# Kernel optimization log

Measured on AMD Instinct MI355X. Metric: run time of the kernel, lower is better.

Reference implementation:

```python
import jax, jax.numpy as jnp
import numpy as np

B, N, DIM = 8, 8192, 512
H, DH = 8, 64
INNER = H * DH
EPS = 1e-5


def setup_inputs() -> dict:
    key = jax.random.key(0)
    ks = jax.random.split(key, 5)
    x = jax.random.normal(ks[0], (B, N, DIM), dtype=jnp.float32)
    w_qkv = jax.random.normal(ks[1], (DIM, 3 * INNER), dtype=jnp.float32) * (DIM ** -0.5)
    ln_w = jnp.ones((INNER,), dtype=jnp.float32)
    ln_b = jnp.zeros((INNER,), dtype=jnp.float32)
    w_out = jax.random.normal(ks[2], (INNER, DIM), dtype=jnp.float32) * (INNER ** -0.5)
    b_out = jnp.zeros((DIM,), dtype=jnp.float32)
    return {"x": x, "w_qkv": w_qkv, "ln_w": ln_w, "ln_b": ln_b,
            "w_out": w_out, "b_out": b_out}


def _layernorm(x, w, b):
    mu = jnp.mean(x, axis=-1, keepdims=True)
    var = jnp.mean(jnp.square(x - mu), axis=-1, keepdims=True)
    return (x - mu) * jax.lax.rsqrt(var + EPS) * w + b


def reference(x, w_qkv, ln_w, ln_b, w_out, b_out):
    b, n, _ = x.shape
    qkv = x @ w_qkv  # [b, n, 3*inner]
    q, k, v = jnp.split(qkv, 3, axis=-1)
    # b n (h d) -> b h n d
    def heads(t):
        return t.reshape(b, n, H, DH).transpose(0, 2, 1, 3)
    q, k, v = heads(q), heads(k), heads(v)
    q = jax.nn.relu(q)
    k = jax.nn.relu(k)
    kv = jnp.einsum('bhnm,bhnd->bhmd', k, v)   # [b, h, d, d]
    out = jnp.einsum('bhnm,bhmd->bhnd', q, kv)  # [b, h, n, d]
    out = out.transpose(0, 2, 1, 3).reshape(b, n, INNER)
    out = _layernorm(out, ln_w, ln_b)
    return out @ w_out + b_out
```

## Files before the change

### kernel.cpp

```cpp
#include <hip/hip_runtime.h>
#include <stdint.h>

#define B_ 8
#define N_ 8192
#define DIM_ 512
#define H_ 8
#define DH_ 64
#define ROWS (B_*N_)
#define TRIPLE (3*DIM_)
#define EPS_ 1e-5f

typedef __attribute__((ext_vector_type(8))) short short8;
typedef __attribute__((ext_vector_type(4))) float f32x4;
typedef __attribute__((ext_vector_type(4))) float fl4;
typedef __attribute__((ext_vector_type(4))) unsigned short us4;
typedef __attribute__((ext_vector_type(8))) unsigned short us8;

#define AS1 __attribute__((address_space(1)))
#define AS3 __attribute__((address_space(3)))

__device__ __forceinline__ void gld16(const void* g, void* l) {
    __builtin_amdgcn_global_load_lds((const AS1 void*)(uintptr_t)g,
                                     (AS3 void*)(unsigned)(uintptr_t)l, 16, 0, 0);
}

__device__ inline unsigned short f2bf(float f) {
    union { float f; unsigned int u; } x; x.f = f;
    unsigned int r = x.u + 0x7fffu + ((x.u >> 16) & 1u);
    return (unsigned short)(r >> 16);
}
__device__ inline float bf2f(unsigned short b) {
    union { unsigned int u; float f; } x; x.u = ((unsigned int)b) << 16;
    return x.f;
}

__device__ __forceinline__ int eoff(int row, int col) {
    return row * 64 + (col ^ ((((unsigned)row >> 2) & 3) << 4));
}

__global__ __launch_bounds__(256) void k_cvt(const float* __restrict__ x,
                                             unsigned short* __restrict__ xb) {
    size_t i = ((size_t)blockIdx.x * 256 + threadIdx.x) * 8;
    fl4 a = *(const fl4*)(x + i);
    fl4 b = *(const fl4*)(x + i + 4);
    us8 r;
    r[0] = f2bf(a[0]); r[1] = f2bf(a[1]); r[2] = f2bf(a[2]); r[3] = f2bf(a[3]);
    r[4] = f2bf(b[0]); r[5] = f2bf(b[1]); r[6] = f2bf(b[2]); r[7] = f2bf(b[3]);
    *(us8*)(xb + i) = r;
}

__global__ __launch_bounds__(256) void k_prep(const float* __restrict__ wq,
        const float* __restrict__ wo,
        unsigned short* __restrict__ wqT, unsigned short* __restrict__ woT) {
    __shared__ float T[32][33];
    int bid = blockIdx.x;
    const float* src; unsigned short* dst; int srcCols, dstCols, k0, n0;
    if (bid < 768) {
        int tn = bid % 48, tk = bid / 48;
        src = wq; dst = wqT; srcCols = 1536; dstCols = 512;
        k0 = tk * 32; n0 = tn * 32;
    } else {
        int b = bid - 768;
        int tn = b % 16, tk = b / 16;
        src = wo; dst = woT; srcCols = 512; dstCols = 512;
        k0 = tk * 32; n0 = tn * 32;
    }
    int t = threadIdx.x, r = t >> 3, c4 = (t & 7) * 4;
    fl4 v = *(const fl4*)(src + (size_t)(k0 + r) * srcCols + n0 + c4);
    T[c4 + 0][r] = v[0]; T[c4 + 1][r] = v[1];
    T[c4 + 2][r] = v[2]; T[c4 + 3][r] = v[3];
    __syncthreads();
    us4 o;
    o[0] = f2bf(T[r][c4 + 0]); o[1] = f2bf(T[r][c4 + 1]);
    o[2] = f2bf(T[r][c4 + 2]); o[3] = f2bf(T[r][c4 + 3]);
    *(us4*)(dst + (size_t)(n0 + r) * dstCols + k0 + c4) = o;
}

__global__ __launch_bounds__(512, 2) void k_qkv8(const unsigned short* __restrict__ xb,
        const unsigned short* __restrict__ wT,
        unsigned short* __restrict__ qkv)
{
    __shared__ __align__(1024) unsigned short Ab[4][8192];
    __shared__ __align__(1024) unsigned short Bb[4][8192];

    const int tid  = threadIdx.x;
    const int lane = tid & 63;
    const int wid  = tid >> 6;
    const int wr   = wid >> 2;
    const int wc   = wid & 3;
    const int lr   = lane & 15;

    int id  = blockIdx.x;
    int nid = (id & 7) * 192 + (id >> 3);
    int n0  = (nid % 6) * 256;
    int m0  = (nid / 6) * 256;

    const unsigned short* pA[2];
    const unsigned short* pB[2];
    unsigned ldst[2];
#pragma unroll
    for (int j = 0; j < 2; ++j) {
        int s    = tid + j * 512;
        int row  = ((s >> 6) << 4) + ((s >> 2) & 15);
        int colb = ((s & 3) << 4) ^ (((s >> 5) & 1) << 5);
        int col  = colb >> 1;
        pA[j] = xb + (size_t)(m0 + row) * 512 + col;
        pB[j] = wT + (size_t)(n0 + row) * 512 + col;
        ldst[j] = (unsigned)((j * 512 + wid * 64) * 8);
    }
    const int kg = (lane >> 4) * 8;
    const int lo = lr * 32 + (kg ^ ((lr >> 3) << 4));

    auto STAGE = [&](int t, int slot) {
#pragma unroll
        for (int j = 0; j < 2; ++j) {
            gld16(pA[j] + t * 32, (void*)&Ab[slot][ldst[j]]);
            gld16(pB[j] + t * 32, (void*)&Bb[slot][ldst[j]]);
        }
    };

    f32x4 acc[8][4] = {};
    short8 af[8], bfr[4];

    STAGE(0, 0);
    STAGE(1, 1);
    STAGE(2, 2);

#define WAITV(n) asm volatile("s_waitcnt vmcnt(" #n ")" ::: "memory")
#pragma unroll
    for (int t = 0; t < 16; ++t) {
        if (t <= 13)      WAITV(8);
        else if (t == 14) WAITV(4);
        else              WAITV(0);
        __builtin_amdgcn_s_barrier();
        __builtin_amdgcn_sched_barrier(0);

        if (t + 3 < 16) STAGE(t + 3, (t + 3) & 3);
        const unsigned short* Ac = Ab[t & 3];
        const unsigned short* Bc = Bb[t & 3];
#pragma unroll
        for (int m = 0; m < 8; ++m)
            af[m] = *(const short8*)&Ac[(wr * 8 + m) * 512 + lo];
#pragma unroll
        for (int n = 0; n < 4; ++n)
            bfr[n] = *(const short8*)&Bc[(wc * 4 + n) * 512 + lo];

        __builtin_amdgcn_s_setprio(1);
#pragma unroll
        for (int m = 0; m < 8; ++m)
#pragma unroll
            for (int n = 0; n < 4; ++n)
                acc[m][n] = __builtin_amdgcn_mfma_f32_16x16x32_bf16(af[m], bfr[n], acc[m][n], 0, 0, 0);
        __builtin_amdgcn_s_setprio(0);
    }
#undef WAITV

    __syncthreads();

    unsigned short* S = (wid < 4) ? (&Ab[0][0] + wid * 8192)
                                  : (&Bb[0][0] + (wid - 4) * 8192);
    const bool relu_tile = (n0 < 1024);
#pragma unroll
    for (int m = 0; m < 8; ++m) {
        int rbase = m * 16 + ((lane >> 4) << 2);
#pragma unroll
        for (int n = 0; n < 4; ++n) {
            int col = n * 16 + lr;
#pragma unroll
            for (int r = 0; r < 4; ++r) {
                float v = acc[m][n][r];
                if (relu_tile && v < 0.0f) v = 0.0f;
                S[eoff(rbase + r, col)] = f2bf(v);
            }
        }
    }
    __syncthreads();
    {
        int rsub = lane >> 3, sub = lane & 7;
        size_t grow = (size_t)(m0 + wr * 128);
        int gcol = n0 + wc * 64 + sub * 8;
#pragma unroll
        for (int rd = 0; rd < 16; ++rd) {
            int row = rd * 8 + rsub;
            short8 vv = *(const short8*)&S[eoff(row, sub * 8)];
            *(short8*)(qkv + (grow + row) * TRIPLE + gcol) = vv;
        }
    }
}

__global__ __launch_bounds__(256) void k_qkv_f(const float* __restrict__ x,
        const unsigned short* __restrict__ wT,
        unsigned short* __restrict__ qkv)
{
    __shared__ unsigned short As[128][40];
    __shared__ unsigned short Bs[128][40];
    int t = threadIdx.x;
    int lane = t & 63, wave = t >> 6;
    int m0 = blockIdx.y * 128;
    int n0 = blockIdx.x * 128;
    int wm = (wave & 1) * 64, wn = (wave >> 1) * 64;
    int lr = lane & 15, kg = (lane >> 4) * 8;

    f32x4 acc[4][4] = {};
    for (int k0 = 0; k0 < DIM_; k0 += 32) {
#pragma unroll
        for (int i = 0; i < 4; ++i) {
            int c = t + 256 * i;
            int r = c >> 3, c4 = (c & 7) * 4;
            fl4 v = *(const fl4*)(x + (size_t)(m0 + r) * DIM_ + k0 + c4);
            unsigned short* dst = &As[r][c4];
            dst[0] = f2bf(v[0]); dst[1] = f2bf(v[1]); dst[2] = f2bf(v[2]); dst[3] = f2bf(v[3]);
        }
#pragma unroll
        for (int i = 0; i < 2; ++i) {
            int c = t + 256 * i;
            int r = c >> 2, c8 = (c & 3) * 8;
            *(int4*)&Bs[r][c8] = *(const int4*)(wT + (size_t)(n0 + r) * DIM_ + k0 + c8);
        }
        __syncthreads();
        short8 af[4], bfr[4];
#pragma unroll
        for (int i = 0; i < 4; ++i) af[i]  = *(short8*)&As[wm + i*16 + lr][kg];
#pragma unroll
        for (int j = 0; j < 4; ++j) bfr[j] = *(short8*)&Bs[wn + j*16 + lr][kg];
#pragma unroll
        for (int i = 0; i < 4; ++i)
#pragma unroll
            for (int j = 0; j < 4; ++j)
                acc[i][j] = __builtin_amdgcn_mfma_f32_16x16x32_bf16(af[i], bfr[j], acc[i][j], 0, 0, 0);
        __syncthreads();
    }
#pragma unroll
    for (int i = 0; i < 4; ++i) {
        int row = m0 + wm + i*16 + (lane >> 4) * 4;
#pragma unroll
        for (int j = 0; j < 4; ++j) {
            int col = n0 + wn + j*16 + (lane & 15);
            bool rl = (col < 1024);
#pragma unroll
            for (int r = 0; r < 4; ++r) {
                float v = acc[i][j][r];
                if (rl && v < 0.0f) v = 0.0f;
                qkv[(size_t)(row + r) * TRIPLE + col] = f2bf(v);
            }
        }
    }
}

__global__ __launch_bounds__(256) void k_kv(const unsigned short* __restrict__ qkv,
                                            float* __restrict__ kv)
{
    __shared__ unsigned short KT[64][136];
    __shared__ unsigned short VT[64][136];
    __shared__ float red[64 * 64];
    int t = threadIdx.x, lane = t & 63, wave = t >> 6;
    int bh = blockIdx.x;
    int b = bh >> 3, h = bh & 7;
    int chunk = blockIdx.y;
    size_t rowbase = (size_t)b * N_ + (size_t)chunk * 1024;
    int kcol = DIM_ + h * 64;
    int vcol = 2 * DIM_ + h * 64;
    int lr = lane & 15;

    f32x4 acc[4][4] = {};
    for (int tile = 0; tile < 8; ++tile) {
        size_t r0 = rowbase + tile * 128;
#pragma unroll
        for (int i = 0; i < 8; ++i) {
            int c = t + 256 * i;
            int r = c >> 4, f4 = (c & 15) * 4;
            us4 kq = *(const us4*)(qkv + (r0 + r) * TRIPLE + kcol + f4);
            us4 vq = *(const us4*)(qkv + (r0 + r) * TRIPLE + vcol + f4);
#pragma unroll
            for (int j = 0; j < 4; ++j) { KT[f4 + j][r] = kq[j]; VT[f4 + j][r] = vq[j]; }
        }
        __syncthreads();
        int kg = wave * 32 + (lane >> 4) * 8;
        short8 af[4], bfr[4];
#pragma unroll
        for (int i = 0; i < 4; ++i) af[i]  = *(short8*)&KT[i*16 + lr][kg];
#pragma unroll
        for (int j = 0; j < 4; ++j) bfr[j] = *(short8*)&VT[j*16 + lr][kg];
#pragma unroll
        for (int i = 0; i < 4; ++i)
#pragma unroll
            for (int j = 0; j < 4; ++j)
                acc[i][j] = __builtin_amdgcn_mfma_f32_16x16x32_bf16(af[i], bfr[j], acc[i][j], 0, 0, 0);
        __syncthreads();
    }
    for (int w = 0; w < 4; ++w) {
        if (wave == w) {
#pragma unroll
            for (int i = 0; i < 4; ++i)
#pragma unroll
                for (int j = 0; j < 4; ++j)
#pragma unroll
                    for (int r = 0; r < 4; ++r) {
                        int m = i*16 + (lane >> 4) * 4 + r;
                        int d = j*16 + (lane & 15);
                        if (w == 0) red[m * 64 + d] = acc[i][j][r];
                        else        red[m * 64 + d] += acc[i][j][r];
                    }
        }
        __syncthreads();
    }
    float* kvout = kv + (size_t)bh * 4096;
#pragma unroll
    for (int i = 0; i < 16; ++i) {
        int idx = t + 256 * i;
        atomicAdd(&kvout[idx], red[idx]);
    }
}

__global__ __launch_bounds__(256) void k_attn(unsigned short* __restrict__ qkv,
                                              const float* __restrict__ kv,
                                              float* __restrict__ rowstats)
{
    __shared__ unsigned short Qh[128][72];
    __shared__ unsigned short kvT[64][72];
    __shared__ __align__(64) unsigned short Sout[128 * 64];
    int t = threadIdx.x, lane = t & 63, wave = t >> 6;
    size_t r0 = (size_t)blockIdx.x * 128;
    int b = (int)(r0 / N_);
    int lr = lane & 15;

    float s8[8] = {}, ss8[8] = {};

    for (int h = 0; h < H_; ++h) {
#pragma unroll
        for (int i = 0; i < 8; ++i) {
            int c = t + 256 * i;
            int r = c >> 4, f4 = (c & 15) * 4;
            *(us4*)&Qh[r][f4] = *(const us4*)(qkv + (r0 + r) * TRIPLE + h * 64 + f4);
        }
        const float* kvh = kv + (size_t)(b * 8 + h) * 4096;
#pragma unroll
        for (int i = 0; i < 16; ++i) {
            int idx = t + 256 * i;
            int m = idx >> 6, d = idx & 63;
            kvT[d][m] = f2bf(kvh[idx]);
        }
        __syncthreads();
        f32x4 acc[2][4] = {};
#pragma unroll
        for (int ks = 0; ks < 2; ++ks) {
            int kg = ks * 32 + (lane >> 4) * 8;
            short8 af[2], bfr[4];
#pragma unroll
            for (int i = 0; i < 2; ++i) af[i]  = *(short8*)&Qh[wave*32 + i*16 + lr][kg];
#pragma unroll
            for (int j = 0; j < 4; ++j) bfr[j] = *(short8*)&kvT[j*16 + lr][kg];
#pragma unroll
            for (int i = 0; i < 2; ++i)
#pragma unroll
                for (int j = 0; j < 4; ++j)
                    acc[i][j] = __builtin_amdgcn_mfma_f32_16x16x32_bf16(af[i], bfr[j], acc[i][j], 0, 0, 0);
        }
#pragma unroll
        for (int i = 0; i < 2; ++i)
#pragma unroll
            for (int j = 0; j < 4; ++j) {
                int rbase = wave*32 + i*16 + (lane >> 4) * 4;
                int col = j*16 + lr;
#pragma unroll
                for (int r = 0; r < 4; ++r) {
                    float v = acc[i][j][r];
                    s8[i*4+r]  += v;
                    ss8[i*4+r] += v * v;
                    Sout[eoff(rbase + r, col)] = f2bf(v);
                }
            }
        __syncthreads();
        {
            int sub = t & 7, rsub = t >> 3;
#pragma unroll
            for (int rd = 0; rd < 4; ++rd) {
                int row = rd * 32 + rsub;
                short8 vv = *(const short8*)&Sout[eoff(row, sub * 8)];
                *(short8*)(qkv + (r0 + row) * TRIPLE + h * 64 + sub * 8) = vv;
            }
        }
        __syncthreads();
    }

#pragma unroll
    for (int q = 0; q < 8; ++q) {
        float s = s8[q], ss = ss8[q];
        s += __shfl_xor(s, 1);  ss += __shfl_xor(ss, 1);
        s += __shfl_xor(s, 2);  ss += __shfl_xor(ss, 2);
        s += __shfl_xor(s, 4);  ss += __shfl_xor(ss, 4);
        s += __shfl_xor(s, 8);  ss += __shfl_xor(ss, 8);
        s8[q] = s; ss8[q] = ss;
    }
    if (lr == 0) {
#pragma unroll
        for (int q = 0; q < 8; ++q) {
            int row = wave*32 + (q >> 2)*16 + (lane >> 4)*4 + (q & 3);
            float m = s8[q] * (1.0f / 512.0f);
            float rs = rsqrtf(ss8[q] * (1.0f / 512.0f) - m * m + EPS_);
            rowstats[2 * (r0 + row)]     = m;
            rowstats[2 * (r0 + row) + 1] = rs;
        }
    }
}

__global__ __launch_bounds__(256) void k_out(const unsigned short* __restrict__ qkv,
        const unsigned short* __restrict__ woutT,
        const float* __restrict__ rowstats,
        const float* __restrict__ lnw, const float* __restrict__ lnb,
        const float* __restrict__ bout, float* __restrict__ out)
{
    __shared__ unsigned short As[128][40];
    __shared__ unsigned short Bs[128][40];
    __shared__ float mu[128], rs[128], lw[512], lb[512];
    int t = threadIdx.x, lane = t & 63, wave = t >> 6;
    int m0 = blockIdx.y * 128, n0 = blockIdx.x * 128;
    int wm = (wave & 1) * 64, wn = (wave >> 1) * 64;
    int lr = lane & 15, kg = (lane >> 4) * 8;

    for (int i = t; i < 512; i += 256) { lw[i] = lnw[i]; lb[i] = lnb[i]; }
    if (t < 128) {
        mu[t] = rowstats[2 * (m0 + t)];
        rs[t] = rowstats[2 * (m0 + t) + 1];
    }
    __syncthreads();

    f32x4 acc[4][4] = {};
    for (int k0 = 0; k0 < 512; k0 += 32) {
#pragma unroll
        for (int i = 0; i < 4; ++i) {
            int c = t + 256 * i;
            int r = c >> 3, c4 = (c & 7) * 4;
            us4 v = *(const us4*)(qkv + (size_t)(m0 + r) * TRIPLE + k0 + c4);
            float mm = mu[r], rr = rs[r];
            unsigned short* dst = &As[r][c4];
#pragma unroll
            for (int j = 0; j < 4; ++j) {
                float f = (bf2f(v[j]) - mm) * rr * lw[k0 + c4 + j] + lb[k0 + c4 + j];
                dst[j] = f2bf(f);
            }
        }
#pragma unroll
        for (int i = 0; i < 2; ++i) {
            int c = t + 256 * i;
            int r = c >> 2, c8 = (c & 3) * 8;
            *(int4*)&Bs[r][c8] = *(const int4*)(woutT + (size_t)(n0 + r) * DIM_ + k0 + c8);
        }
        __syncthreads();
        short8 af[4], bfr[4];
#pragma unroll
        for (int i = 0; i < 4; ++i) af[i]  = *(short8*)&As[wm + i*16 + lr][kg];
#pragma unroll
        for (int j = 0; j < 4; ++j) bfr[j] = *(short8*)&Bs[wn + j*16 + lr][kg];
#pragma unroll
        for (int i = 0; i < 4; ++i)
#pragma unroll
            for (int j = 0; j < 4; ++j)
                acc[i][j] = __builtin_amdgcn_mfma_f32_16x16x32_bf16(af[i], bfr[j], acc[i][j], 0, 0, 0);
        __syncthreads();
    }
#pragma unroll
    for (int i = 0; i < 4; ++i) {
        int row = m0 + wm + i*16 + (lane >> 4) * 4;
#pragma unroll
        for (int j = 0; j < 4; ++j) {
            int col = n0 + wn + j*16 + (lane & 15);
            float bo = bout[col];
#pragma unroll
            for (int r = 0; r < 4; ++r)
                out[(size_t)(row + r) * DIM_ + col] = acc[i][j][r] + bo;
        }
    }
}

extern "C" void kernel_launch(void* const* d_in, const int* in_sizes, int n_in,
                              void* d_out, int out_size, void* d_ws, size_t ws_size,
                              hipStream_t stream) {
    (void)in_sizes; (void)n_in; (void)out_size;
    const float* x     = (const float*)d_in[0];
    const float* w_qkv = (const float*)d_in[1];
    const float* ln_w  = (const float*)d_in[2];
    const float* ln_b  = (const float*)d_in[3];
    const float* w_out = (const float*)d_in[4];
    const float* b_out = (const float*)d_in[5];
    float* out = (float*)d_out;

    char* ws = (char*)d_ws;
    const size_t QKV_BYTES = (size_t)ROWS * TRIPLE * sizeof(unsigned short);
    const size_t KV_BYTES  = (size_t)64 * 64 * 64 * sizeof(float);
    const size_t WQT_BYTES = (size_t)TRIPLE * DIM_ * sizeof(unsigned short);
    const size_t WOT_BYTES = (size_t)DIM_ * DIM_ * sizeof(unsigned short);
    const size_t RS_BYTES  = (size_t)ROWS * 2 * sizeof(float);
    const size_t XB_BYTES  = (size_t)ROWS * DIM_ * sizeof(unsigned short);
    unsigned short* qkv   = (unsigned short*)ws;
    float*          kvbuf = (float*)(ws + QKV_BYTES);
    unsigned short* wqkvT = (unsigned short*)(ws + QKV_BYTES + KV_BYTES);
    unsigned short* woutT = (unsigned short*)(ws + QKV_BYTES + KV_BYTES + WQT_BYTES);
    float*          rstat = (float*)(ws + QKV_BYTES + KV_BYTES + WQT_BYTES + WOT_BYTES);
    unsigned short* xb    = (unsigned short*)(ws + QKV_BYTES + KV_BYTES + WQT_BYTES + WOT_BYTES + RS_BYTES);
    const size_t NEED = QKV_BYTES + KV_BYTES + WQT_BYTES + WOT_BYTES + RS_BYTES + XB_BYTES;

    hipMemsetAsync(kvbuf, 0, KV_BYTES, stream);
    k_prep<<<1024, 256, 0, stream>>>(w_qkv, w_out, wqkvT, woutT);
    if (ws_size >= NEED) {
        k_cvt<<<16384, 256, 0, stream>>>(x, xb);
        k_qkv8<<<dim3(1536), 512, 0, stream>>>(xb, wqkvT, qkv);
    } else {
        k_qkv_f<<<dim3(12, 512), 256, 0, stream>>>(x, wqkvT, qkv);
    }
    k_kv<<<dim3(64, 8), 256, 0, stream>>>(qkv, kvbuf);
    k_attn<<<512, 256, 0, stream>>>(qkv, kvbuf, rstat);
    k_out<<<dim3(4, 512), 256, 0, stream>>>(qkv, woutT, rstat, ln_w, ln_b, b_out, out);
}
```

Baseline: 552.5 us.

## Shrink QKV GEMM tile to 256x128 with 3-stage pipeline for higher occupancy

The bf16 QKV projection kernel moves from 256x256 output tiles with a 4-deep LDS ring to 256x128 tiles with a 3-deep ring in one unified LDS buffer. Launch bounds go from 2 to 4 blocks per SM and the grid doubles to 3072 blocks. The aim is more resident waves to hide latency, paid for with lower arithmetic intensity per tile (more A re-reads from memory) and a shallower prefetch depth.

```diff
diff --git a/kernel.cpp b/kernel.cpp
--- a/kernel.cpp
+++ b/kernel.cpp
@@ -76,78 +76,78 @@
     *(us4*)(dst + (size_t)(n0 + r) * dstCols + k0 + c4) = o;
 }
 
-__global__ __launch_bounds__(512, 2) void k_qkv8(const unsigned short* __restrict__ xb,
+__global__ __launch_bounds__(512, 4) void k_qkv8(const unsigned short* __restrict__ xb,
         const unsigned short* __restrict__ wT,
         unsigned short* __restrict__ qkv)
 {
-    __shared__ __align__(1024) unsigned short Ab[4][8192];
-    __shared__ __align__(1024) unsigned short Bb[4][8192];
+    __shared__ __align__(1024) unsigned short LDSb[3][12288];
 
     const int tid  = threadIdx.x;
     const int lane = tid & 63;
     const int wid  = tid >> 6;
-    const int wr   = wid >> 2;
-    const int wc   = wid & 3;
+    const int wr   = wid >> 1;
+    const int wc   = wid & 1;
     const int lr   = lane & 15;
 
     int id  = blockIdx.x;
-    int nid = (id & 7) * 192 + (id >> 3);
-    int n0  = (nid % 6) * 256;
-    int m0  = (nid / 6) * 256;
+    int nid = (id & 7) * 384 + (id >> 3);
+    int n0  = (nid % 12) * 128;
+    int m0  = (nid / 12) * 256;
 
     const unsigned short* pA[2];
-    const unsigned short* pB[2];
-    unsigned ldst[2];
+    const unsigned short* pB1;
+    unsigned ldstA[2], ldstB;
 #pragma unroll
     for (int j = 0; j < 2; ++j) {
         int s    = tid + j * 512;
         int row  = ((s >> 6) << 4) + ((s >> 2) & 15);
         int colb = ((s & 3) << 4) ^ (((s >> 5) & 1) << 5);
-        int col  = colb >> 1;
-        pA[j] = xb + (size_t)(m0 + row) * 512 + col;
-        pB[j] = wT + (size_t)(n0 + row) * 512 + col;
-        ldst[j] = (unsigned)((j * 512 + wid * 64) * 8);
+        pA[j] = xb + (size_t)(m0 + row) * 512 + (colb >> 1);
+        ldstA[j] = (unsigned)((j * 512 + wid * 64) * 8);
+    }
+    {
+        int s    = tid;
+        int row  = ((s >> 6) << 4) + ((s >> 2) & 15);
+        int colb = ((s & 3) << 4) ^ (((s >> 5) & 1) << 5);
+        pB1 = wT + (size_t)(n0 + row) * 512 + (colb >> 1);
+        ldstB = (unsigned)(8192 + wid * 64 * 8);
     }
     const int kg = (lane >> 4) * 8;
     const int lo = lr * 32 + (kg ^ ((lr >> 3) << 4));
 
     auto STAGE = [&](int t, int slot) {
-#pragma unroll
-        for (int j = 0; j < 2; ++j) {
-            gld16(pA[j] + t * 32, (void*)&Ab[slot][ldst[j]]);
-            gld16(pB[j] + t * 32, (void*)&Bb[slot][ldst[j]]);
-        }
+        gld16(pA[0] + t * 32, (void*)&LDSb[slot][ldstA[0]]);
+        gld16(pA[1] + t * 32, (void*)&LDSb[slot][ldstA[1]]);
+        gld16(pB1   + t * 32, (void*)&LDSb[slot][ldstB]);
     };
 
-    f32x4 acc[8][4] = {};
-    short8 af[8], bfr[4];
+    f32x4 acc[4][4] = {};
+    short8 af[4], bfr[4];
 
     STAGE(0, 0);
     STAGE(1, 1);
-    STAGE(2, 2);
 
 #define WAITV(n) asm volatile("s_waitcnt vmcnt(" #n ")" ::: "memory")
 #pragma unroll
     for (int t = 0; t < 16; ++t) {
-        if (t <= 13)      WAITV(8);
-        else if (t == 14) WAITV(4);
-        else              WAITV(0);
+        if (t <= 14) WAITV(3);
+        else         WAITV(0);
         __builtin_amdgcn_s_barrier();
         __builtin_amdgcn_sched_barrier(0);
 
-        if (t + 3 < 16) STAGE(t + 3, (t + 3) & 3);
-        const unsigned short* Ac = Ab[t & 3];
-        const unsigned short* Bc = Bb[t & 3];
-#pragma unroll
-        for (int m = 0; m < 8; ++m)
-            af[m] = *(const short8*)&Ac[(wr * 8 + m) * 512 + lo];
+        if (t + 2 < 16) STAGE(t + 2, (t + 2) % 3);
+
+        const unsigned short* L = LDSb[t % 3];
+#pragma unroll
+        for (int m = 0; m < 4; ++m)
+            af[m] = *(const short8*)&L[(wr * 4 + m) * 512 + lo];
 #pragma unroll
         for (int n = 0; n < 4; ++n)
-            bfr[n] = *(const short8*)&Bc[(wc * 4 + n) * 512 + lo];
+            bfr[n] = *(const short8*)&L[8192 + (wc * 4 + n) * 512 + lo];
 
         __builtin_amdgcn_s_setprio(1);
 #pragma unroll
-        for (int m = 0; m < 8; ++m)
+        for (int m = 0; m < 4; ++m)
 #pragma unroll
             for (int n = 0; n < 4; ++n)
                 acc[m][n] = __builtin_amdgcn_mfma_f32_16x16x32_bf16(af[m], bfr[n], acc[m][n], 0, 0, 0);
@@ -157,11 +157,10 @@
 
     __syncthreads();
 
-    unsigned short* S = (wid < 4) ? (&Ab[0][0] + wid * 8192)
-                                  : (&Bb[0][0] + (wid - 4) * 8192);
+    unsigned short* S = ((unsigned short*)LDSb) + wid * 4096;
     const bool relu_tile = (n0 < 1024);
 #pragma unroll
-    for (int m = 0; m < 8; ++m) {
+    for (int m = 0; m < 4; ++m) {
         int rbase = m * 16 + ((lane >> 4) << 2);
 #pragma unroll
         for (int n = 0; n < 4; ++n) {
@@ -177,10 +176,10 @@
     __syncthreads();
     {
         int rsub = lane >> 3, sub = lane & 7;
-        size_t grow = (size_t)(m0 + wr * 128);
+        size_t grow = (size_t)(m0 + wr * 64);
         int gcol = n0 + wc * 64 + sub * 8;
 #pragma unroll
-        for (int rd = 0; rd < 16; ++rd) {
+        for (int rd = 0; rd < 8; ++rd) {
             int row = rd * 8 + rsub;
             short8 vv = *(const short8*)&S[eoff(row, sub * 8)];
             *(short8*)(qkv + (grow + row) * TRIPLE + gcol) = vv;
@@ -504,7 +503,7 @@
     k_prep<<<1024, 256, 0, stream>>>(w_qkv, w_out, wqkvT, woutT);
     if (ws_size >= NEED) {
         k_cvt<<<16384, 256, 0, stream>>>(x, xb);
-        k_qkv8<<<dim3(1536), 512, 0, stream>>>(xb, wqkvT, qkv);
+        k_qkv8<<<dim3(3072), 512, 0, stream>>>(xb, wqkvT, qkv);
     } else {
         k_qkv_f<<<dim3(12, 512), 256, 0, stream>>>(x, wqkvT, qkv);
     }
```

Result: no change. 544.7 us (-1.4%).
